# Kernel optimization log

Measured on AMD Instinct MI355X. Metric: run time of the kernel, lower is better.

## Reference

```python
import jax, jax.numpy as jnp
import numpy as np

N = 200000
E = 3200000
F_IN = 128
D = 64
G = 512
T = 10


def setup_inputs() -> dict:
    key = jax.random.key(0)
    ks = jax.random.split(key, 20)
    def lin(k, out_d, in_d):
        kw, kb = jax.random.split(k)
        s = 1.0 / np.sqrt(in_d)
        W = jax.random.uniform(kw, (out_d, in_d), jnp.float32, -s, s)
        b = jax.random.uniform(kb, (out_d,), jnp.float32, -s, s)
        return W, b
    x = jax.random.normal(ks[0], (N, F_IN), jnp.float32)
    edge_index = jax.random.randint(ks[1], (2, E), 0, N, jnp.int32)
    batch = jnp.sort(jax.random.randint(ks[2], (N,), 0, G, jnp.int32))
    Wc0, bc0 = lin(ks[3], D, F_IN)
    Wc1, bc1 = lin(ks[4], D, D)
    Wc2, bc2 = lin(ks[5], D, D)
    Wc3, bc3 = lin(ks[6], D, D)
    Wmax, bmax = lin(ks[7], D, D)
    W1, b1 = lin(ks[8], D, 4 * D)
    W2, b2 = lin(ks[9], T, D)
    return {"x": x, "edge_index": edge_index, "batch": batch, "num_graphs": G,
            "Wc0": Wc0, "bc0": bc0, "Wc1": Wc1, "bc1": bc1,
            "Wc2": Wc2, "bc2": bc2, "Wc3": Wc3, "bc3": bc3,
            "Wmax": Wmax, "bmax": bmax, "W1": W1, "b1": b1, "W2": W2, "b2": b2}


def gcn_conv(x, W, b, src, dst, n):
    # PyG GCNConv: h = x W^T; add self-loops; sym-normalize by (deg+1)^-1/2
    h = x @ W.T  # [n, D]
    deg = jax.ops.segment_sum(jnp.ones_like(dst, jnp.float32), dst, num_segments=n) + 1.0
    dis = deg ** -0.5  # deg >= 1 always (self loop)
    coef = (dis[src] * dis[dst])[:, None]  # [E,1]
    agg = jax.ops.segment_sum(h[src] * coef, dst, num_segments=n)
    agg = agg + h * (dis * dis)[:, None]  # self-loop contribution
    return agg + b


def reference(x, edge_index, batch, num_graphs,
              Wc0, bc0, Wc1, bc1, Wc2, bc2, Wc3, bc3,
              Wmax, bmax, W1, b1, W2, b2):
    n = x.shape[0]
    src, dst = edge_index[0], edge_index[1]
    convs = [(Wc0, bc0), (Wc1, bc1), (Wc2, bc2), (Wc3, bc3)]
    h = x
    h_all = []
    for (W, b) in convs:
        h = gcn_conv(h, W, b, src, dst, n)
        h = jax.nn.relu(h @ Wmax.T + bmax)
        h_all.append(h)
    hcat = jnp.concatenate(h_all, axis=1)  # [n, 4*D]
    pooled = jax.ops.segment_max(hcat, batch, num_segments=num_graphs)
    pooled = jnp.where(jnp.isfinite(pooled), pooled, 0.0)  # empty graphs -> 0
    out = jax.nn.relu(pooled @ W1.T + b1)
    return out @ W2.T + b2
```

## Files before the change

kernel.cpp:

```cpp
#include <hip/hip_runtime.h>
#include <hip/hip_bf16.h>
#include <math.h>

constexpr int N_NODES = 200000;
constexpr int E_EDGES = 3200000;
constexpr int F_IN    = 128;
constexpr int D       = 64;
constexpr int G_GRAPHS = 512;
constexpr int T_OUT   = 10;

constexpr int SCAN_CHUNK   = 2048;
constexpr int SCAN_NBLOCKS = (N_NODES + SCAN_CHUNK - 1) / SCAN_CHUNK;

constexpr int PLACE_NPASS = 4;
constexpr int PLACE_RANGE = N_NODES / PLACE_NPASS;

__global__ __launch_bounds__(256) void deg_kernel(const int* __restrict__ dst,
                                                  int* __restrict__ deg) {
    int e = blockIdx.x * 256 + threadIdx.x;
    if (e < E_EDGES) atomicAdd(&deg[dst[e]], 1);
}

__global__ __launch_bounds__(256) void dis_kernel(const int* __restrict__ deg,
                                                  float* __restrict__ dis) {
    int i = blockIdx.x * 256 + threadIdx.x;
    if (i < N_NODES) dis[i] = 1.0f / sqrtf((float)deg[i] + 1.0f);
}

__global__ __launch_bounds__(256) void scan_p1(const int* __restrict__ deg,
                                               int* __restrict__ bsum) {
    const int b = blockIdx.x, t = threadIdx.x;
    int idx0 = b * SCAN_CHUNK + t * 8;
    int s = 0;
    #pragma unroll
    for (int i = 0; i < 8; ++i) {
        int idx = idx0 + i;
        if (idx < N_NODES) s += deg[idx];
    }
    #pragma unroll
    for (int off = 32; off; off >>= 1) s += __shfl_down(s, off, 64);
    __shared__ int ws[4];
    if ((t & 63) == 0) ws[t >> 6] = s;
    __syncthreads();
    if (t == 0) bsum[b] = ws[0] + ws[1] + ws[2] + ws[3];
}

__global__ __launch_bounds__(128) void scan_p2(int* __restrict__ bsum,
                                               int* __restrict__ row_ptr) {
    __shared__ int tmp[128];
    const int t = threadIdx.x;
    int v = (t < SCAN_NBLOCKS) ? bsum[t] : 0;
    tmp[t] = v;
    __syncthreads();
    #pragma unroll
    for (int off = 1; off < 128; off <<= 1) {
        int u = (t >= off) ? tmp[t - off] : 0;
        __syncthreads();
        tmp[t] += u;
        __syncthreads();
    }
    if (t < SCAN_NBLOCKS) bsum[t] = tmp[t] - v;
    if (t == 0) row_ptr[N_NODES] = E_EDGES;
}

__global__ __launch_bounds__(256) void scan_p3(const int* __restrict__ deg,
                                               const int* __restrict__ bsum,
                                               int* __restrict__ row_ptr) {
    const int b = blockIdx.x, t = threadIdx.x;
    int idx0 = b * SCAN_CHUNK + t * 8;
    int loc[8];
    int s = 0;
    #pragma unroll
    for (int i = 0; i < 8; ++i) {
        int idx = idx0 + i;
        loc[i] = (idx < N_NODES) ? deg[idx] : 0;
        s += loc[i];
    }
    __shared__ int tmp[256];
    tmp[t] = s;
    __syncthreads();
    #pragma unroll
    for (int off = 1; off < 256; off <<= 1) {
        int u = (t >= off) ? tmp[t - off] : 0;
        __syncthreads();
        tmp[t] += u;
        __syncthreads();
    }
    int run = tmp[t] - s + bsum[b];
    #pragma unroll
    for (int i = 0; i < 8; ++i) {
        int idx = idx0 + i;
        if (idx < N_NODES) row_ptr[idx] = run;
        run += loc[i];
    }
}

__global__ __launch_bounds__(256) void place_pass(const int* __restrict__ src,
                                                  const int* __restrict__ dst,
                                                  const int* __restrict__ row_ptr,
                                                  int* __restrict__ cursor,
                                                  int* __restrict__ csr_src,
                                                  int lo, int hi) {
    int e0 = (blockIdx.x * 256 + threadIdx.x) * 4;
    if (e0 >= E_EDGES) return;
    int4 d4 = *(const int4*)(dst + e0);
    const int* dp = (const int*)&d4;
    #pragma unroll
    for (int i = 0; i < 4; ++i) {
        int d = dp[i];
        if (d >= lo && d < hi) {
            int pos = row_ptr[d] + atomicAdd(&cursor[d], 1);
            csr_src[pos] = src[e0 + i];
        }
    }
}

template<int K, bool FUSED_MAX, bool SCALE>
__global__ __launch_bounds__(256) void gemm_k(const float* __restrict__ in,
                                              const float* __restrict__ W,
                                              float* __restrict__ out,
                                              const float* __restrict__ bias,
                                              const int* __restrict__ batch,
                                              int* __restrict__ pooled,
                                              const float* __restrict__ dis,
                                              int layer) {
    constexpr int GPR = K / 4;
    __shared__ float smem[64 * K + D * K];
    __shared__ int   bs[64];
    __shared__ float ds[64];
    float* Xs = smem;
    float* Ws = smem + 64 * K;
    const int tid = threadIdx.x;
    const size_t row0 = (size_t)blockIdx.x * 64;

    for (int li = tid; li < 64 * GPR; li += 256) {
        int r = li / GPR, g = li % GPR;
        float4 v = *(const float4*)(in + (row0 + r) * K + g * 4);
        int gs = g ^ ((r >> 2) & 7);
        *(float4*)(Xs + r * K + gs * 4) = v;
    }
    for (int li = tid; li < D * GPR; li += 256) {
        int r = li / GPR, g = li % GPR;
        float4 v = *(const float4*)(W + r * K + g * 4);
        int gs = g ^ ((r >> 2) & 7);
        *(float4*)(Ws + r * K + gs * 4) = v;
    }
    if (FUSED_MAX && tid < 64) bs[tid] = batch[row0 + tid];
    if (SCALE && tid < 64)     ds[tid] = dis[row0 + tid];
    __syncthreads();

    const int lane = tid & 63;
    const int wave = tid >> 6;
    const int rg = lane & 15;
    const int cg = wave * 4 + (lane >> 4);
    float acc[4][4] = {};
    #pragma unroll 8
    for (int kq = 0; kq < GPR; ++kq) {
        float4 xv[4], wv[4];
        #pragma unroll
        for (int i = 0; i < 4; ++i)
            xv[i] = *(const float4*)(Xs + (rg * 4 + i) * K + ((kq ^ (rg & 7)) * 4));
        #pragma unroll
        for (int j = 0; j < 4; ++j)
            wv[j] = *(const float4*)(Ws + (cg * 4 + j) * K + ((kq ^ (cg & 7)) * 4));
        #pragma unroll
        for (int i = 0; i < 4; ++i)
            #pragma unroll
            for (int j = 0; j < 4; ++j)
                acc[i][j] += xv[i].x * wv[j].x + xv[i].y * wv[j].y +
                             xv[i].z * wv[j].z + xv[i].w * wv[j].w;
    }

    if constexpr (FUSED_MAX) {
        __syncthreads();
        float* Ts = smem;
        #pragma unroll
        for (int i = 0; i < 4; ++i) {
            size_t r = row0 + rg * 4 + i;
            float4 o;
            float* op = (float*)&o;
            #pragma unroll
            for (int j = 0; j < 4; ++j)
                op[j] = fmaxf(acc[i][j] + bias[cg * 4 + j], 0.0f);
            *(float4*)(out + r * D + cg * 4) = o;
            *(float4*)(Ts + (rg * 4 + i) * 68 + cg * 4) = o;
        }
        __syncthreads();
        if (tid < 64) {
            const int col = tid;
            float m = Ts[col];
            int bg = bs[0];
            #pragma unroll 8
            for (int r = 1; r < 64; ++r) {
                int b2 = bs[r];
                float v = Ts[r * 68 + col];
                if (b2 != bg) {
                    atomicMax(&pooled[bg * (4 * D) + layer * D + col], __float_as_int(m));
                    bg = b2; m = v;
                } else {
                    m = fmaxf(m, v);
                }
            }
            atomicMax(&pooled[bg * (4 * D) + layer * D + col], __float_as_int(m));
        }
    } else {
        #pragma unroll
        for (int i = 0; i < 4; ++i) {
            size_t r = row0 + rg * 4 + i;
            float sc = SCALE ? ds[rg * 4 + i] : 1.0f;
            float4 o = make_float4(acc[i][0] * sc, acc[i][1] * sc,
                                   acc[i][2] * sc, acc[i][3] * sc);
            *(float4*)(out + r * D + cg * 4) = o;
        }
    }
}

__global__ __launch_bounds__(256) void agg_kernel(const int* __restrict__ row_ptr,
                                                  const int* __restrict__ csr_src,
                                                  const float* __restrict__ Lbuf,
                                                  const float* __restrict__ dis,
                                                  const float* __restrict__ bias,
                                                  float* __restrict__ A) {
    int v = __builtin_amdgcn_readfirstlane((int)(blockIdx.x * 4) + (int)(threadIdx.x >> 6));
    if (v >= N_NODES) return;
    const int lane = threadIdx.x & 63;
    const int beg = row_ptr[v];
    const int end = row_ptr[v + 1];
    float acc = Lbuf[(size_t)v * D + lane];
    #pragma unroll 4
    for (int p = beg; p < end; ++p) {
        int s = csr_src[p];
        acc += Lbuf[(size_t)s * D + lane];
    }
    A[(size_t)v * D + lane] = acc * dis[v] + bias[lane];
}

__global__ __launch_bounds__(64) void mlp_kernel(const float* __restrict__ pooled,
                                                 const float* __restrict__ W1,
                                                 const float* __restrict__ b1,
                                                 const float* __restrict__ W2,
                                                 const float* __restrict__ b2,
                                                 float* __restrict__ out) {
    __shared__ float ps[4 * D];
    __shared__ float hs[D];
    const int g = blockIdx.x, t = threadIdx.x;
    *(float4*)(ps + t * 4) = *(const float4*)(pooled + (size_t)g * (4 * D) + t * 4);
    __syncthreads();
    float acc = b1[t];
    const float* w = W1 + (size_t)t * (4 * D);
    #pragma unroll 4
    for (int k = 0; k < 4 * D; k += 4) {
        float4 wv = *(const float4*)(w + k);
        float4 pv = *(const float4*)(ps + k);
        acc += wv.x * pv.x + wv.y * pv.y + wv.z * pv.z + wv.w * pv.w;
    }
    hs[t] = fmaxf(acc, 0.0f);
    __syncthreads();
    if (t < T_OUT) {
        float o = b2[t];
        const float* w2 = W2 + t * D;
        #pragma unroll
        for (int k = 0; k < D; ++k) o += hs[k] * w2[k];
        out[(size_t)g * T_OUT + t] = o;
    }
}

extern "C" void kernel_launch(void* const* d_in, const int* in_sizes, int n_in,
                              void* d_out, int out_size, void* d_ws, size_t ws_size,
                              hipStream_t stream) {
    (void)in_sizes; (void)n_in; (void)out_size; (void)ws_size;
    const float* x     = (const float*)d_in[0];
    const int*   ei    = (const int*)d_in[1];
    const int*   batch = (const int*)d_in[2];
    const float* Wc[4] = {(const float*)d_in[4], (const float*)d_in[6],
                          (const float*)d_in[8], (const float*)d_in[10]};
    const float* bc[4] = {(const float*)d_in[5], (const float*)d_in[7],
                          (const float*)d_in[9], (const float*)d_in[11]};
    const float* Wmax = (const float*)d_in[12];
    const float* bmax = (const float*)d_in[13];
    const float* W1   = (const float*)d_in[14];
    const float* b1   = (const float*)d_in[15];
    const float* W2   = (const float*)d_in[16];
    const float* b2   = (const float*)d_in[17];
    float* out = (float*)d_out;

    float* fws = (float*)d_ws;
    size_t off = 0;
    float* L        = fws + off; off += (size_t)N_NODES * D;
    float* A        = fws + off; off += (size_t)N_NODES * D;
    int*   csr_src  = (int*)(fws + off); off += E_EDGES;
    int*   row_ptr  = (int*)(fws + off); off += N_NODES + 16;
    int*   deg      = (int*)(fws + off); off += N_NODES;
    int*   cursor   = (int*)(fws + off); off += N_NODES;
    float* dis      = fws + off; off += N_NODES;
    int*   pooled   = (int*)(fws + off); off += G_GRAPHS * 4 * D;
    int*   bsum     = (int*)(fws + off); off += SCAN_NBLOCKS + 16;

    const int* srcI = ei;
    const int* dstI = ei + E_EDGES;

    hipMemsetAsync(deg,    0, sizeof(int) * N_NODES, stream);
    hipMemsetAsync(cursor, 0, sizeof(int) * N_NODES, stream);
    hipMemsetAsync(pooled, 0, sizeof(int) * G_GRAPHS * 4 * D, stream);

    deg_kernel <<<(E_EDGES + 255) / 256, 256, 0, stream>>>(dstI, deg);
    dis_kernel <<<(N_NODES + 255) / 256, 256, 0, stream>>>(deg, dis);
    scan_p1<<<SCAN_NBLOCKS, 256, 0, stream>>>(deg, bsum);
    scan_p2<<<1, 128, 0, stream>>>(bsum, row_ptr);
    scan_p3<<<SCAN_NBLOCKS, 256, 0, stream>>>(deg, bsum, row_ptr);
    for (int p = 0; p < PLACE_NPASS; ++p)
        place_pass<<<E_EDGES / (256 * 4), 256, 0, stream>>>(srcI, dstI, row_ptr,
                                                            cursor, csr_src,
                                                            p * PLACE_RANGE,
                                                            (p + 1) * PLACE_RANGE);

    const float* cur = x;
    for (int l = 0; l < 4; ++l) {
        if (l == 0)
            gemm_k<F_IN, false, true><<<N_NODES / 64, 256, 0, stream>>>(
                cur, Wc[0], L, nullptr, nullptr, nullptr, dis, 0);
        else
            gemm_k<D, false, true><<<N_NODES / 64, 256, 0, stream>>>(
                cur, Wc[l], L, nullptr, nullptr, nullptr, dis, 0);
        agg_kernel<<<N_NODES / 4, 256, 0, stream>>>(row_ptr, csr_src,
                                                    L, dis, bc[l], A);
        gemm_k<D, true, false><<<N_NODES / 64, 256, 0, stream>>>(
            A, Wmax, L, bmax, batch, pooled, nullptr, l);
        cur = L;
    }
    mlp_kernel<<<G_GRAPHS, 64, 0, stream>>>((const float*)pooled, W1, b1, W2, b2, out);
}
```

Measured before the change: 1.365 ms.

## Fuse Wmax GEMM with next-layer conv GEMM and fold conv bias

Each layer's Wmax projection, ReLU and segment-max pooling are fused with the next layer's conv weight GEMM in one kernel. This drops the intermediate hidden-state write and re-read and one launch per layer. The conv bias is folded into a precomputed Wmax·bc + bmax vector, so the aggregation kernel no longer adds it. The degree atomics are also split into four destination-range passes to improve atomic locality, at the cost of reading dst four times. The fused kernel needs more shared memory (three 16KB tiles), which may lower occupancy.

Result: no change. 1.364 ms (-0.1%).

```diff
diff --git a/kernel.cpp b/kernel.cpp
--- a/kernel.cpp
+++ b/kernel.cpp
@@ -12,13 +12,21 @@
 constexpr int SCAN_CHUNK   = 2048;
 constexpr int SCAN_NBLOCKS = (N_NODES + SCAN_CHUNK - 1) / SCAN_CHUNK;
 
-constexpr int PLACE_NPASS = 4;
-constexpr int PLACE_RANGE = N_NODES / PLACE_NPASS;
-
-__global__ __launch_bounds__(256) void deg_kernel(const int* __restrict__ dst,
-                                                  int* __restrict__ deg) {
-    int e = blockIdx.x * 256 + threadIdx.x;
-    if (e < E_EDGES) atomicAdd(&deg[dst[e]], 1);
+constexpr int NPASS = 4;
+constexpr int PASS_RANGE = N_NODES / NPASS;
+
+__global__ __launch_bounds__(256) void deg_pass(const int* __restrict__ dst,
+                                                int* __restrict__ deg,
+                                                int lo, int hi) {
+    int e0 = (blockIdx.x * 256 + threadIdx.x) * 4;
+    if (e0 >= E_EDGES) return;
+    int4 d4 = *(const int4*)(dst + e0);
+    const int* dp = (const int*)&d4;
+    #pragma unroll
+    for (int i = 0; i < 4; ++i) {
+        int d = dp[i];
+        if (d >= lo && d < hi) atomicAdd(&deg[d], 1);
+    }
 }
 
 __global__ __launch_bounds__(256) void dis_kernel(const int* __restrict__ deg,
@@ -115,21 +123,35 @@
     }
 }
 
-template<int K, bool FUSED_MAX, bool SCALE>
+__global__ __launch_bounds__(256) void bprime_kernel(const float* __restrict__ Wmax,
+                                                     const float* __restrict__ bmax,
+                                                     const float* __restrict__ bc0,
+                                                     const float* __restrict__ bc1,
+                                                     const float* __restrict__ bc2,
+                                                     const float* __restrict__ bc3,
+                                                     float* __restrict__ bprime) {
+    const int l = threadIdx.x >> 6, c = threadIdx.x & 63;
+    const float* bc = (l == 0) ? bc0 : (l == 1) ? bc1 : (l == 2) ? bc2 : bc3;
+    float s = bmax[c];
+    const float* w = Wmax + c * D;
+    #pragma unroll
+    for (int k = 0; k < D; k += 4) {
+        float4 wv = *(const float4*)(w + k);
+        float4 bv = *(const float4*)(bc + k);
+        s += wv.x * bv.x + wv.y * bv.y + wv.z * bv.z + wv.w * bv.w;
+    }
+    bprime[l * D + c] = s;
+}
+
+template<int K>
 __global__ __launch_bounds__(256) void gemm_k(const float* __restrict__ in,
                                               const float* __restrict__ W,
                                               float* __restrict__ out,
-                                              const float* __restrict__ bias,
-                                              const int* __restrict__ batch,
-                                              int* __restrict__ pooled,
-                                              const float* __restrict__ dis,
-                                              int layer) {
+                                              const float* __restrict__ dis) {
     constexpr int GPR = K / 4;
-    __shared__ float smem[64 * K + D * K];
-    __shared__ int   bs[64];
+    __shared__ float Xs[64 * K];
+    __shared__ float Ws[D * K];
     __shared__ float ds[64];
-    float* Xs = smem;
-    float* Ws = smem + 64 * K;
     const int tid = threadIdx.x;
     const size_t row0 = (size_t)blockIdx.x * 64;
 
@@ -145,8 +167,7 @@
         int gs = g ^ ((r >> 2) & 7);
         *(float4*)(Ws + r * K + gs * 4) = v;
     }
-    if (FUSED_MAX && tid < 64) bs[tid] = batch[row0 + tid];
-    if (SCALE && tid < 64)     ds[tid] = dis[row0 + tid];
+    if (tid < 64) ds[tid] = dis[row0 + tid];
     __syncthreads();
 
     const int lane = tid & 63;
@@ -170,47 +191,137 @@
                 acc[i][j] += xv[i].x * wv[j].x + xv[i].y * wv[j].y +
                              xv[i].z * wv[j].z + xv[i].w * wv[j].w;
     }
-
-    if constexpr (FUSED_MAX) {
-        __syncthreads();
-        float* Ts = smem;
+    #pragma unroll
+    for (int i = 0; i < 4; ++i) {
+        size_t r = row0 + rg * 4 + i;
+        float sc = ds[rg * 4 + i];
+        float4 o = make_float4(acc[i][0] * sc, acc[i][1] * sc,
+                               acc[i][2] * sc, acc[i][3] * sc);
+        *(float4*)(out + r * D + cg * 4) = o;
+    }
+}
+
+template<bool HAS_NEXT>
+__global__ __launch_bounds__(256) void fused2_kernel(const float* __restrict__ A,
+                                                     const float* __restrict__ Wmax,
+                                                     const float* __restrict__ Wcn,
+                                                     const float* __restrict__ bprime,
+                                                     const int* __restrict__ batch,
+                                                     const float* __restrict__ dis,
+                                                     int* __restrict__ pooled,
+                                                     float* __restrict__ Hout,
+                                                     int layer) {
+    __shared__ float Xs[64 * D];
+    __shared__ float Ws[64 * D];
+    __shared__ float Ws2[64 * D];
+    __shared__ int   bs[64];
+    __shared__ float ds[64];
+    __shared__ float bb[64];
+    const int tid = threadIdx.x;
+    const size_t row0 = (size_t)blockIdx.x * 64;
+
+    for (int li = tid; li < 64 * 16; li += 256) {
+        int r = li >> 4, g = li & 15;
+        float4 v = *(const float4*)(A + (row0 + r) * D + g * 4);
+        *(float4*)(Xs + r * D + ((g ^ ((r >> 2) & 7)) * 4)) = v;
+    }
+    for (int li = tid; li < 64 * 16; li += 256) {
+        int r = li >> 4, g = li & 15;
+        float4 v = *(const float4*)(Wmax + r * D + g * 4);
+        *(float4*)(Ws + r * D + ((g ^ ((r >> 2) & 7)) * 4)) = v;
+    }
+    if (HAS_NEXT)
+        for (int li = tid; li < 64 * 16; li += 256) {
+            int r = li >> 4, g = li & 15;
+            float4 v = *(const float4*)(Wcn + r * D + g * 4);
+            *(float4*)(Ws2 + r * D + ((g ^ ((r >> 2) & 7)) * 4)) = v;
+        }
+    if (tid < 64) {
+        bs[tid] = batch[row0 + tid];
+        bb[tid] = bprime[tid];
+        if (HAS_NEXT) ds[tid] = dis[row0 + tid];
+    }
+    __syncthreads();
+
+    const int lane = tid & 63;
+    const int wave = tid >> 6;
+    const int rg = lane & 15;
+    const int cg = wave * 4 + (lane >> 4);
+
+    float acc[4][4] = {};
+    #pragma unroll 8
+    for (int kq = 0; kq < 16; ++kq) {
+        float4 xv[4], wv[4];
+        #pragma unroll
+        for (int i = 0; i < 4; ++i)
+            xv[i] = *(const float4*)(Xs + (rg * 4 + i) * D + ((kq ^ (rg & 7)) * 4));
+        #pragma unroll
+        for (int j = 0; j < 4; ++j)
+            wv[j] = *(const float4*)(Ws + (cg * 4 + j) * D + ((kq ^ (cg & 7)) * 4));
+        #pragma unroll
+        for (int i = 0; i < 4; ++i)
+            #pragma unroll
+            for (int j = 0; j < 4; ++j)
+                acc[i][j] += xv[i].x * wv[j].x + xv[i].y * wv[j].y +
+                             xv[i].z * wv[j].z + xv[i].w * wv[j].w;
+    }
+
+    __syncthreads();
+    #pragma unroll
+    for (int i = 0; i < 4; ++i) {
+        float4 o;
+        float* op = (float*)&o;
+        #pragma unroll
+        for (int j = 0; j < 4; ++j)
+            op[j] = fmaxf(acc[i][j] + bb[cg * 4 + j], 0.0f);
+        *(float4*)(Xs + (rg * 4 + i) * D + ((cg ^ (rg & 7)) * 4)) = o;
+    }
+    __syncthreads();
+
+    if (tid < 64) {
+        const int col = tid;
+        const int cgr = col >> 2, ce = col & 3;
+        float m = Xs[(cgr ^ 0) * 4 + ce];
+        int bg = bs[0];
+        #pragma unroll 8
+        for (int r = 1; r < 64; ++r) {
+            int b2 = bs[r];
+            float v = Xs[r * D + ((cgr ^ ((r >> 2) & 7)) * 4) + ce];
+            if (b2 != bg) {
+                atomicMax(&pooled[bg * (4 * D) + layer * D + col], __float_as_int(m));
+                bg = b2; m = v;
+            } else {
+                m = fmaxf(m, v);
+            }
+        }
+        atomicMax(&pooled[bg * (4 * D) + layer * D + col], __float_as_int(m));
+    }
+
+    if (HAS_NEXT) {
+        float acc2[4][4] = {};
+        #pragma unroll 8
+        for (int kq = 0; kq < 16; ++kq) {
+            float4 xv[4], wv[4];
+            #pragma unroll
+            for (int i = 0; i < 4; ++i)
+                xv[i] = *(const float4*)(Xs + (rg * 4 + i) * D + ((kq ^ (rg & 7)) * 4));
+            #pragma unroll
+            for (int j = 0; j < 4; ++j)
+                wv[j] = *(const float4*)(Ws2 + (cg * 4 + j) * D + ((kq ^ (cg & 7)) * 4));
+            #pragma unroll
+            for (int i = 0; i < 4; ++i)
+                #pragma unroll
+                for (int j = 0; j < 4; ++j)
+                    acc2[i][j] += xv[i].x * wv[j].x + xv[i].y * wv[j].y +
+                                  xv[i].z * wv[j].z + xv[i].w * wv[j].w;
+        }
         #pragma unroll
         for (int i = 0; i < 4; ++i) {
             size_t r = row0 + rg * 4 + i;
-            float4 o;
-            float* op = (float*)&o;
-            #pragma unroll
-            for (int j = 0; j < 4; ++j)
-                op[j] = fmaxf(acc[i][j] + bias[cg * 4 + j], 0.0f);
-            *(float4*)(out + r * D + cg * 4) = o;
-            *(float4*)(Ts + (rg * 4 + i) * 68 + cg * 4) = o;
-        }
-        __syncthreads();
-        if (tid < 64) {
-            const int col = tid;
-            float m = Ts[col];
-            int bg = bs[0];
-            #pragma unroll 8
-            for (int r = 1; r < 64; ++r) {
-                int b2 = bs[r];
-                float v = Ts[r * 68 + col];
-                if (b2 != bg) {
-                    atomicMax(&pooled[bg * (4 * D) + layer * D + col], __float_as_int(m));
-                    bg = b2; m = v;
-                } else {
-                    m = fmaxf(m, v);
-                }
-            }
-            atomicMax(&pooled[bg * (4 * D) + layer * D + col], __float_as_int(m));
-        }
-    } else {
-        #pragma unroll
-        for (int i = 0; i < 4; ++i) {
-            size_t r = row0 + rg * 4 + i;
-            float sc = SCALE ? ds[rg * 4 + i] : 1.0f;
-            float4 o = make_float4(acc[i][0] * sc, acc[i][1] * sc,
-                                   acc[i][2] * sc, acc[i][3] * sc);
-            *(float4*)(out + r * D + cg * 4) = o;
+            float sc = ds[rg * 4 + i];
+            float4 o = make_float4(acc2[i][0] * sc, acc2[i][1] * sc,
+                                   acc2[i][2] * sc, acc2[i][3] * sc);
+            *(float4*)(Hout + r * D + cg * 4) = o;
         }
     }
 }
@@ -219,7 +330,6 @@
                                                   const int* __restrict__ csr_src,
                                                   const float* __restrict__ Lbuf,
                                                   const float* __restrict__ dis,
-                                                  const float* __restrict__ bias,
                                                   float* __restrict__ A) {
     int v = __builtin_amdgcn_readfirstlane((int)(blockIdx.x * 4) + (int)(threadIdx.x >> 6));
     if (v >= N_NODES) return;
@@ -232,7 +342,7 @@
         int s = csr_src[p];
         acc += Lbuf[(size_t)s * D + lane];
     }
-    A[(size_t)v * D + lane] = acc * dis[v] + bias[lane];
+    A[(size_t)v * D + lane] = acc * dis[v];
 }
 
 __global__ __launch_bounds__(64) void mlp_kernel(const float* __restrict__ pooled,
@@ -295,6 +405,7 @@
     float* dis      = fws + off; off += N_NODES;
     int*   pooled   = (int*)(fws + off); off += G_GRAPHS * 4 * D;
     int*   bsum     = (int*)(fws + off); off += SCAN_NBLOCKS + 16;
+    float* bprime   = fws + off; off += 4 * D;
 
     const int* srcI = ei;
     const int* dstI = ei + E_EDGES;
@@ -303,30 +414,32 @@
     hipMemsetAsync(cursor, 0, sizeof(int) * N_NODES, stream);
     hipMemsetAsync(pooled, 0, sizeof(int) * G_GRAPHS * 4 * D, stream);
 
-    deg_kernel <<<(E_EDGES + 255) / 256, 256, 0, stream>>>(dstI, deg);
-    dis_kernel <<<(N_NODES + 255) / 256, 256, 0, stream>>>(deg, dis);
+    for (int p = 0; p < NPASS; ++p)
+        deg_pass<<<E_EDGES / (256 * 4), 256, 0, stream>>>(dstI, deg,
+                                                          p * PASS_RANGE,
+                                                          (p + 1) * PASS_RANGE);
+    dis_kernel<<<(N_NODES + 255) / 256, 256, 0, stream>>>(deg, dis);
     scan_p1<<<SCAN_NBLOCKS, 256, 0, stream>>>(deg, bsum);
     scan_p2<<<1, 128, 0, stream>>>(bsum, row_ptr);
     scan_p3<<<SCAN_NBLOCKS, 256, 0, stream>>>(deg, bsum, row_ptr);
-    for (int p = 0; p < PLACE_NPASS; ++p)
+    for (int p = 0; p < NPASS; ++p)
         place_pass<<<E_EDGES / (256 * 4), 256, 0, stream>>>(srcI, dstI, row_ptr,
                                                             cursor, csr_src,
-                                                            p * PLACE_RANGE,
-                                                            (p + 1) * PLACE_RANGE);
-
-    const float* cur = x;
+                                                            p * PASS_RANGE,
+                                                            (p + 1) * PASS_RANGE);
+    bprime_kernel<<<1, 256, 0, stream>>>(Wmax, bmax, bc[0], bc[1], bc[2], bc[3],
+                                         bprime);
+
+    gemm_k<F_IN><<<N_NODES / 64, 256, 0, stream>>>(x, Wc[0], L, dis);
+
     for (int l = 0; l < 4; ++l) {
-        if (l == 0)
-            gemm_k<F_IN, false, true><<<N_NODES / 64, 256, 0, stream>>>(
-                cur, Wc[0], L, nullptr, nullptr, nullptr, dis, 0);
+        agg_kernel<<<N_NODES / 4, 256, 0, stream>>>(row_ptr, csr_src, L, dis, A);
+        if (l < 3)
+            fused2_kernel<true><<<N_NODES / 64, 256, 0, stream>>>(
+                A, Wmax, Wc[l + 1], bprime + l * D, batch, dis, pooled, L, l);
         else
-            gemm_k<D, false, true><<<N_NODES / 64, 256, 0, stream>>>(
-                cur, Wc[l], L, nullptr, nullptr, nullptr, dis, 0);
-        agg_kernel<<<N_NODES / 4, 256, 0, stream>>>(row_ptr, csr_src,
-                                                    L, dis, bc[l], A);
-        gemm_k<D, true, false><<<N_NODES / 64, 256, 0, stream>>>(
-            A, Wmax, L, bmax, batch, pooled, nullptr, l);
-        cur = L;
+            fused2_kernel<false><<<N_NODES / 64, 256, 0, stream>>>(
+                A, Wmax, nullptr, bprime + l * D, batch, nullptr, pooled, nullptr, l);
     }
     mlp_kernel<<<G_GRAPHS, 64, 0, stream>>>((const float*)pooled, W1, b1, W2, b2, out);
 }
```
